# Performance work log

Hardware: AMD Instinct MI355X
Metric: run time of the kernel (lower is better)

The kernel has to match this reference:

```python
import jax, jax.numpy as jnp
import numpy as np

H_DIM = 64
GRID = 8
NBR = 2.0
BN_EPS = 1e-5
N_SEQ = 64
N_PED = 64
BOTTLENECK = 1024


def setup_inputs() -> dict:
    key = jax.random.key(0)
    k0, k1, k2, k3 = jax.random.split(key, 4)
    batch = N_SEQ * N_PED
    h_states = jax.random.normal(k0, (1, batch, H_DIM), jnp.float32)
    # positions spread over a 4x4 area so some neighbors fall inside the 2.0 neighborhood
    end_pos = jax.random.uniform(k1, (batch, 2), jnp.float32) * 4.0
    rel_pos = jax.random.normal(k2, (batch, 2), jnp.float32)
    starts = jnp.arange(N_SEQ, dtype=jnp.int32) * N_PED
    seq_start_end = jnp.stack([starts, starts + N_PED], axis=1)
    in_dim = GRID * GRID * H_DIM  # 4096
    W = jax.random.normal(k3, (in_dim, BOTTLENECK), jnp.float32) / np.sqrt(in_dim)
    b = jnp.zeros((BOTTLENECK,), jnp.float32)
    gamma = jnp.ones((BOTTLENECK,), jnp.float32)
    beta = jnp.zeros((BOTTLENECK,), jnp.float32)
    return {"h_states": h_states, "seq_start_end": seq_start_end, "end_pos": end_pos,
            "rel_pos": rel_pos, "W": W, "b": b, "gamma": gamma, "beta": beta}


def _pool_scene(hidden, pos):
    # hidden: (n, h), pos: (n, 2). Pair (i, j): ped j binned into ped i's grid.
    n, h = hidden.shape
    g2 = GRID * GRID
    half = NBR / 2.0
    tl_x = pos[:, 0] - half
    tl_y = pos[:, 1] + half
    br_x = pos[:, 0] + half
    br_y = pos[:, 1] - half
    px = pos[None, :, 0]  # (1, n) -> broadcast over i
    py = pos[None, :, 1]
    cell_x = jnp.floor((px - tl_x[:, None]) / NBR * GRID)
    cell_y = jnp.floor((tl_y[:, None] - py) / NBR * GRID)
    grid = (cell_x + cell_y * GRID).astype(jnp.int32) + 1  # slot 0 = trash bin
    oob = ((px >= br_x[:, None]) | (px <= tl_x[:, None]) |
           (py >= tl_y[:, None]) | (py <= br_y[:, None]) |
           jnp.eye(n, dtype=bool))  # self-interaction excluded
    grid = grid + (jnp.arange(n, dtype=jnp.int32) * g2)[:, None]
    grid = jnp.where(oob, 0, grid)  # (n, n)
    src = jnp.broadcast_to(hidden[None], (n, n, h)).reshape(-1, h)
    buf = jnp.zeros((n * g2 + 1, h), hidden.dtype).at[grid.reshape(-1)].add(src)
    return buf[1:].reshape(n, g2 * h)


def reference(h_states, seq_start_end, end_pos, rel_pos, W, b, gamma, beta):
    batch = end_pos.shape[0]
    n_seq = seq_start_end.shape[0]
    n_ped = batch // n_seq  # equal-length scenes by construction
    hid = h_states.reshape(-1, H_DIM).reshape(n_seq, n_ped, H_DIM)
    pos = end_pos.reshape(n_seq, n_ped, 2)
    pool_h = jax.vmap(_pool_scene)(hid, pos).reshape(batch, -1)  # (batch, 4096)
    x = pool_h @ W + b
    # BatchNorm1d in training mode (batch statistics, biased variance)
    mean = jnp.mean(x, axis=0)
    var = jnp.var(x, axis=0)
    x = (x - mean) * jax.lax.rsqrt(var + BN_EPS) * gamma + beta
    return jax.nn.relu(x)
```

## Files before the change

kernel.cpp:

```cpp
#include <hip/hip_runtime.h>
#include <hip/hip_bf16.h>


#define NPED  64
#define BATCH 4096
#define HDIM  64
#define G2    64
#define KDIM  4096
#define NOUT  1024

typedef __attribute__((ext_vector_type(8))) short short8;
typedef __attribute__((ext_vector_type(4))) float f32x4;

__device__ __forceinline__ unsigned short f2bf(float f) {
    __hip_bfloat16 h = __float2bfloat16(f);
    return *reinterpret_cast<unsigned short*>(&h);
}

__device__ __forceinline__ void lds_load16(const void* g, void* l) {
    __builtin_amdgcn_global_load_lds(
        (const __attribute__((address_space(1))) void*)g,
        (__attribute__((address_space(3))) void*)l, 16, 0, 0);
}

__global__ __launch_bounds__(512) void pool_kernel(const float* __restrict__ h,
                                                   const float* __restrict__ pos,
                                                   unsigned short* __restrict__ A2) {
    __shared__ float hs[NPED * HDIM];
    __shared__ float pl[NPED * 2];
    int t = threadIdx.x;
    int w = t >> 6, lane = t & 63;
    int p0 = blockIdx.x * 8;
    int sbase = p0 & ~(NPED - 1);
    if (t < 128) pl[t] = pos[sbase * 2 + t];
    {
        const float4* src = (const float4*)(h + (size_t)sbase * HDIM);
        float4* dst = (float4*)hs;
        dst[t] = src[t];
        dst[t + 512] = src[t + 512];
    }
    __syncthreads();

    int i = p0 + w;
    int il = i & (NPED - 1);
    float cx0 = pl[2 * il], cy0 = pl[2 * il + 1];
    float tlx = cx0 - 1.f, tly = cy0 + 1.f, brx = cx0 + 1.f, bry = cy0 - 1.f;
    float px = pl[2 * lane], py = pl[2 * lane + 1];
    bool inb = (lane != il) && !(px >= brx || px <= tlx || py >= tly || py <= bry);
    int cellx = (int)floorf((px - tlx) * 4.f);
    int celly = (int)floorf((tly - py) * 4.f);
    int cell = cellx + celly * 8;
    inb = inb && ((unsigned)cell < 64u);

    int mtile = i >> 4, r = i & 15;
    unsigned short* outb = A2 + (size_t)mtile * 65536 + r * 8
                              + (lane >> 5) * 512 + ((lane >> 3) & 3) * 128 + (lane & 7);
    const float* hrow = hs + lane;
    #pragma unroll
    for (int c = 0; c < 64; ++c) {
        unsigned long long m = __ballot(inb && (cell == c));
        float a = 0.f;
        while (m) {
            int j = __builtin_ctzll(m);
            m &= m - 1;
            a += hrow[j * HDIM];
        }
        outb[c * 1024] = f2bf(a);
    }
}

__global__ __launch_bounds__(256) void wt_kernel(const float* __restrict__ W,
                                                 unsigned short* __restrict__ Wt,
                                                 float* __restrict__ stats) {
    __shared__ unsigned short tile[64][66];
    int k0 = blockIdx.x * 64;
    int n0 = blockIdx.y * 64;
    int t = threadIdx.x;
    if (blockIdx.x == 0 && blockIdx.y < 8) stats[blockIdx.y * 256 + t] = 0.f;
    #pragma unroll
    for (int p = 0; p < 4; ++p) {
        int lin = p * 256 + t;
        int c4 = lin & 15, kl = lin >> 4;
        float4 v = ((const float4*)(W + (size_t)(k0 + kl) * NOUT + n0))[c4];
        tile[c4 * 4 + 0][kl] = f2bf(v.x);
        tile[c4 * 4 + 1][kl] = f2bf(v.y);
        tile[c4 * 4 + 2][kl] = f2bf(v.z);
        tile[c4 * 4 + 3][kl] = f2bf(v.w);
    }
    __syncthreads();
    unsigned int* out = (unsigned int*)Wt;
    #pragma unroll
    for (int p = 0; p < 8; ++p) {
        int lin = p * 256 + t;
        int ku = lin & 31, nl = lin >> 5;
        unsigned int v = (unsigned int)tile[nl][2 * ku] |
                         ((unsigned int)tile[nl][2 * ku + 1] << 16);
        out[(size_t)(n0 + nl) * (KDIM / 2) + (k0 >> 1) + ku] = v;
    }
}

__global__ __launch_bounds__(256, 2) void gemm_kernel(const unsigned short* __restrict__ A2,
                                                      const unsigned short* __restrict__ Bt,
                                                      float* __restrict__ C,
                                                      float* __restrict__ P1,
                                                      float* __restrict__ P2,
                                                      float* __restrict__ P3) {
    __shared__ __align__(16) unsigned short Bs[128 * 64];
    int t = threadIdx.x;
    int w = t >> 6, lane = t & 63;
    int m0 = blockIdx.x * 256, n0 = blockIdx.y * 128;
    int kbase = blockIdx.z * 1024;
    int wm = w * 64;

    f32x4 acc[4][8];
    #pragma unroll
    for (int i = 0; i < 4; ++i)
        #pragma unroll
        for (int j = 0; j < 8; ++j)
            acc[i][j] = (f32x4){0.f, 0.f, 0.f, 0.f};

    int rbase = w * 32 + (lane >> 3);
    int koff = ((lane & 7) ^ (lane >> 3)) * 8;
    const unsigned short* Bg = Bt + (size_t)(n0 + rbase) * KDIM + kbase + koff;
    unsigned short* BsW = Bs + w * 2048 + lane * 8;

    const unsigned short* Abase = A2 + (size_t)((m0 + wm) >> 4) * 65536 + lane * 8;
    int ktile0 = kbase >> 5;

    for (int kt = 0; kt < 1024; kt += 64) {
        #pragma unroll
        for (int q = 0; q < 4; ++q)
            lds_load16(Bg + (size_t)q * 8 * KDIM + kt, BsW + q * 512);
        short8 af[2][4];
        int ktile = ktile0 + (kt >> 5);
        #pragma unroll
        for (int kk = 0; kk < 2; ++kk)
            #pragma unroll
            for (int i = 0; i < 4; ++i)
                af[kk][i] = *(const short8*)(Abase + ((size_t)i * 128 + ktile + kk) * 512);
        __syncthreads();
        #pragma unroll
        for (int kk = 0; kk < 2; ++kk) {
            int chunk = ((kk * 4 + (lane >> 4)) ^ (lane & 7)) * 8;
            #pragma unroll
            for (int j = 0; j < 8; ++j) {
                short8 b = *(const short8*)&Bs[(j * 16 + (lane & 15)) * 64 + chunk];
                #pragma unroll
                for (int i = 0; i < 4; ++i)
                    acc[i][j] = __builtin_amdgcn_mfma_f32_16x16x32_bf16(af[kk][i], b, acc[i][j], 0, 0, 0);
            }
        }
        __syncthreads();
    }

    float* dst = blockIdx.z == 0 ? C : blockIdx.z == 1 ? P1 : blockIdx.z == 2 ? P2 : P3;
    int col0 = n0 + (lane & 15);
    int row0 = m0 + wm + ((lane >> 4) << 2);
    #pragma unroll
    for (int i = 0; i < 4; ++i)
        #pragma unroll
        for (int j = 0; j < 8; ++j)
            #pragma unroll
            for (int r = 0; r < 4; ++r)
                dst[(size_t)(row0 + i * 16 + r) * NOUT + col0 + j * 16] = acc[i][j][r];
}

__global__ __launch_bounds__(256) void combine_stats(float* __restrict__ C,
                                                     const float* __restrict__ P1,
                                                     const float* __restrict__ P2,
                                                     const float* __restrict__ P3,
                                                     float* __restrict__ stats) {
    int t = threadIdx.x;
    int colchunk = blockIdx.x & 3;
    int rowchunk = blockIdx.x >> 2;
    int col = colchunk * 256 + t;
    size_t base = (size_t)rowchunk * 32 * NOUT + col;
    float s = 0.f, s2 = 0.f;
    #pragma unroll 4
    for (int r = 0; r < 32; ++r) {
        size_t ix = base + (size_t)r * NOUT;
        float v = (C[ix] + P1[ix]) + (P2[ix] + P3[ix]);
        C[ix] = v;
        s += v; s2 += v * v;
    }
    atomicAdd(&stats[col], s);
    atomicAdd(&stats[NOUT + col], s2);
}

__global__ __launch_bounds__(256) void norm_kernel(float* __restrict__ C,
                                                   const float* __restrict__ stats,
                                                   const float* __restrict__ gamma,
                                                   const float* __restrict__ beta) {
    int idx = blockIdx.x * 256 + threadIdx.x;
    int col4 = idx & 255;
    float4 x = ((const float4*)C)[idx];
    float4 s = ((const float4*)stats)[col4];
    float4 q = ((const float4*)(stats + NOUT))[col4];
    float4 g = ((const float4*)gamma)[col4];
    float4 b = ((const float4*)beta)[col4];
    const float inv_n = 1.f / 4096.f;
    float m, inv;
    m = s.x * inv_n; inv = rsqrtf(q.x * inv_n - m * m + 1e-5f); x.x = fmaxf((x.x - m) * inv * g.x + b.x, 0.f);
    m = s.y * inv_n; inv = rsqrtf(q.y * inv_n - m * m + 1e-5f); x.y = fmaxf((x.y - m) * inv * g.y + b.y, 0.f);
    m = s.z * inv_n; inv = rsqrtf(q.z * inv_n - m * m + 1e-5f); x.z = fmaxf((x.z - m) * inv * g.z + b.z, 0.f);
    m = s.w * inv_n; inv = rsqrtf(q.w * inv_n - m * m + 1e-5f); x.w = fmaxf((x.w - m) * inv * g.w + b.w, 0.f);
    ((float4*)C)[idx] = x;
}

extern "C" void kernel_launch(void* const* d_in, const int* in_sizes, int n_in,
                              void* d_out, int out_size, void* d_ws, size_t ws_size,
                              hipStream_t stream) {
    const float* h      = (const float*)d_in[0];
    const float* endpos = (const float*)d_in[2];
    const float* W      = (const float*)d_in[4];
    const float* gamma  = (const float*)d_in[6];
    const float* beta   = (const float*)d_in[7];
    float* C = (float*)d_out;

    char* ws = (char*)d_ws;
    size_t off = 0;
    unsigned short* A2 = (unsigned short*)(ws + off); off += (size_t)BATCH * KDIM * 2;
    unsigned short* Wt = (unsigned short*)(ws + off); off += (size_t)NOUT * KDIM * 2;
    float* P1 = (float*)(ws + off); off += (size_t)BATCH * NOUT * 4;
    float* P2 = (float*)(ws + off); off += (size_t)BATCH * NOUT * 4;
    float* P3 = (float*)(ws + off); off += (size_t)BATCH * NOUT * 4;
    float* stats = (float*)(ws + off);

    pool_kernel<<<BATCH / 8, 512, 0, stream>>>(h, endpos, A2);
    wt_kernel<<<dim3(KDIM / 64, NOUT / 64), 256, 0, stream>>>(W, Wt, stats);
    gemm_kernel<<<dim3(BATCH / 256, NOUT / 128, 4), 256, 0, stream>>>(A2, Wt, C, P1, P2, P3);
    combine_stats<<<512, 256, 0, stream>>>(C, P1, P2, P3, stats);
    norm_kernel<<<(BATCH * NOUT / 4) / 256, 256, 0, stream>>>(C, stats, gamma, beta);
}
```

Measured before the change: 149.9 us.

## Fuse split-K reduction and BN stats into GEMM via per-tile completion flags

Drops the separate combine_stats kernel. The z=0 split-K block now spin-waits on a per-tile atomic flag until the other three K-slices have written their partials, then adds them to its own registers, writes C, and accumulates column sums and sums of squares with wave shuffles and atomics. This removes one full pass that wrote C and read it back, plus a kernel launch. The risk is a deadlock or stall if the z=0 blocks take the resident slots before their producer blocks are scheduled, since the 512 blocks may not all be resident at once.

Result: slower. 165.8 us (+10.6%).

```diff
diff --git a/kernel.cpp b/kernel.cpp
--- a/kernel.cpp
+++ b/kernel.cpp
@@ -71,12 +71,14 @@
 
 __global__ __launch_bounds__(256) void wt_kernel(const float* __restrict__ W,
                                                  unsigned short* __restrict__ Wt,
-                                                 float* __restrict__ stats) {
+                                                 float* __restrict__ stats,
+                                                 unsigned int* __restrict__ flags) {
     __shared__ unsigned short tile[64][66];
     int k0 = blockIdx.x * 64;
     int n0 = blockIdx.y * 64;
     int t = threadIdx.x;
     if (blockIdx.x == 0 && blockIdx.y < 8) stats[blockIdx.y * 256 + t] = 0.f;
+    if (blockIdx.x == 1 && blockIdx.y == 0 && t < 128) flags[t] = 0u;
     #pragma unroll
     for (int p = 0; p < 4; ++p) {
         int lin = p * 256 + t;
@@ -104,7 +106,9 @@
                                                       float* __restrict__ C,
                                                       float* __restrict__ P1,
                                                       float* __restrict__ P2,
-                                                      float* __restrict__ P3) {
+                                                      float* __restrict__ P3,
+                                                      float* __restrict__ stats,
+                                                      unsigned int* __restrict__ flags) {
     __shared__ __align__(16) unsigned short Bs[128 * 64];
     int t = threadIdx.x;
     int w = t >> 6, lane = t & 63;
@@ -153,38 +157,47 @@
         __syncthreads();
     }
 
-    float* dst = blockIdx.z == 0 ? C : blockIdx.z == 1 ? P1 : blockIdx.z == 2 ? P2 : P3;
+    int tile = blockIdx.y * 16 + blockIdx.x;
     int col0 = n0 + (lane & 15);
     int row0 = m0 + wm + ((lane >> 4) << 2);
-    #pragma unroll
-    for (int i = 0; i < 4; ++i)
-        #pragma unroll
-        for (int j = 0; j < 8; ++j)
-            #pragma unroll
-            for (int r = 0; r < 4; ++r)
-                dst[(size_t)(row0 + i * 16 + r) * NOUT + col0 + j * 16] = acc[i][j][r];
-}
-
-__global__ __launch_bounds__(256) void combine_stats(float* __restrict__ C,
-                                                     const float* __restrict__ P1,
-                                                     const float* __restrict__ P2,
-                                                     const float* __restrict__ P3,
-                                                     float* __restrict__ stats) {
-    int t = threadIdx.x;
-    int colchunk = blockIdx.x & 3;
-    int rowchunk = blockIdx.x >> 2;
-    int col = colchunk * 256 + t;
-    size_t base = (size_t)rowchunk * 32 * NOUT + col;
-    float s = 0.f, s2 = 0.f;
-    #pragma unroll 4
-    for (int r = 0; r < 32; ++r) {
-        size_t ix = base + (size_t)r * NOUT;
-        float v = (C[ix] + P1[ix]) + (P2[ix] + P3[ix]);
-        C[ix] = v;
-        s += v; s2 += v * v;
-    }
-    atomicAdd(&stats[col], s);
-    atomicAdd(&stats[NOUT + col], s2);
+
+    if (blockIdx.z != 0) {
+        float* dst = blockIdx.z == 1 ? P1 : blockIdx.z == 2 ? P2 : P3;
+        #pragma unroll
+        for (int i = 0; i < 4; ++i)
+            #pragma unroll
+            for (int j = 0; j < 8; ++j)
+                #pragma unroll
+                for (int r = 0; r < 4; ++r)
+                    dst[(size_t)(row0 + i * 16 + r) * NOUT + col0 + j * 16] = acc[i][j][r];
+        asm volatile("s_waitcnt vmcnt(0)" ::: "memory");
+        __syncthreads();
+        if (t == 0) atomicAdd(&flags[tile], 1u);
+    } else {
+        if (t == 0) {
+            while (atomicAdd(&flags[tile], 0u) < 3u) __builtin_amdgcn_s_sleep(8);
+        }
+        __syncthreads();
+        #pragma unroll
+        for (int j = 0; j < 8; ++j) {
+            float s = 0.f, s2 = 0.f;
+            #pragma unroll
+            for (int i = 0; i < 4; ++i)
+                #pragma unroll
+                for (int r = 0; r < 4; ++r) {
+                    size_t ix = (size_t)(row0 + i * 16 + r) * NOUT + col0 + j * 16;
+                    float v = (acc[i][j][r] + P1[ix]) + (P2[ix] + P3[ix]);
+                    C[ix] = v;
+                    s += v; s2 += v * v;
+                }
+            s  += __shfl_xor(s, 16);  s  += __shfl_xor(s, 32);
+            s2 += __shfl_xor(s2, 16); s2 += __shfl_xor(s2, 32);
+            if (lane < 16) {
+                atomicAdd(&stats[col0 + j * 16], s);
+                atomicAdd(&stats[NOUT + col0 + j * 16], s2);
+            }
+        }
+    }
 }
 
 __global__ __launch_bounds__(256) void norm_kernel(float* __restrict__ C,
@@ -224,11 +237,11 @@
     float* P1 = (float*)(ws + off); off += (size_t)BATCH * NOUT * 4;
     float* P2 = (float*)(ws + off); off += (size_t)BATCH * NOUT * 4;
     float* P3 = (float*)(ws + off); off += (size_t)BATCH * NOUT * 4;
-    float* stats = (float*)(ws + off);
+    float* stats = (float*)(ws + off); off += 2 * NOUT * 4;
+    unsigned int* flags = (unsigned int*)(ws + off);
 
     pool_kernel<<<BATCH / 8, 512, 0, stream>>>(h, endpos, A2);
-    wt_kernel<<<dim3(KDIM / 64, NOUT / 64), 256, 0, stream>>>(W, Wt, stats);
-    gemm_kernel<<<dim3(BATCH / 256, NOUT / 128, 4), 256, 0, stream>>>(A2, Wt, C, P1, P2, P3);
-    combine_stats<<<512, 256, 0, stream>>>(C, P1, P2, P3, stats);
+    wt_kernel<<<dim3(KDIM / 64, NOUT / 64), 256, 0, stream>>>(W, Wt, stats, flags);
+    gemm_kernel<<<dim3(BATCH / 256, NOUT / 128, 4), 256, 0, stream>>>(A2, Wt, C, P1, P2, P3, stats, flags);
     norm_kernel<<<(BATCH * NOUT / 4) / 256, 256, 0, stream>>>(C, stats, gamma, beta);
 }
```
